# Optimization experiments

Measured on AMD Instinct MI355X. Metric: run time of the kernel, lower is better.

Reference implementation:

```python
import jax, jax.numpy as jnp
import numpy as np
import math

M = 8                      # multiplicity (channels per irrep)
COMBOS = [(0,0,0),(0,1,1),(1,0,1),(1,1,0),(1,1,1),(2,1,1)]  # (edge_l, node_l, out_l)

def _cg_coeff(j1, m1, j2, m2, j3, m3):
    # standard (Racah) complex Clebsch-Gordan coefficient <j1 m1 j2 m2 | j3 m3>
    if m3 != m1 + m2:
        return 0.0
    f = math.factorial
    vmin = max(0, j2 - j3 - m1, j1 + m2 - j3)
    vmax = min(j1 + j2 - j3, j1 - m1, j2 + m2)
    pref = (2*j3 + 1) * f(j3+j1-j2) * f(j3-j1+j2) * f(j1+j2-j3) / f(j1+j2+j3+1)
    pref *= f(j3+m3) * f(j3-m3) * f(j1-m1) * f(j1+m1) * f(j2-m2) * f(j2+m2)
    s = 0.0
    for v in range(vmin, vmax + 1):
        s += (-1)**v / (f(v) * f(j1+j2-j3-v) * f(j1-m1-v) * f(j2+m2-v)
                        * f(j3-j2+m1+v) * f(j3-j1-m2+v))
    return math.sqrt(pref) * s

def _su2_cg(l1, l2, l3):
    C = np.zeros((2*l1+1, 2*l2+1, 2*l3+1), dtype=np.complex128)
    for m1 in range(-l1, l1+1):
        for m2 in range(-l2, l2+1):
            m3 = m1 + m2
            if -l3 <= m3 <= l3:
                C[m1+l1, m2+l2, m3+l3] = _cg_coeff(l1, m1, l2, m2, l3, m3)
    return C

def _qmat(l):
    # real -> complex spherical-harmonic change of basis (e3nn convention)
    q = np.zeros((2*l+1, 2*l+1), dtype=np.complex128)
    for m in range(-l, 0):
        q[l+m, l+abs(m)] = 1/np.sqrt(2)
        q[l+m, l-abs(m)] = -1j/np.sqrt(2)
    q[l, l] = 1.0
    for m in range(1, l+1):
        q[l+m, l+abs(m)] = (-1)**m / np.sqrt(2)
        q[l+m, l-abs(m)] = 1j * (-1)**m / np.sqrt(2)
    return (-1j)**l * q

def _so3_cg(l1, l2, l3):
    # real-basis CG, normalized to unit Frobenius norm (matches e3nn _so3_clebsch_gordan)
    C = np.einsum('ij,kl,mn,ikn->jlm', _qmat(l1), _qmat(l2),
                  np.conj(_qmat(l3)).T, _su2_cg(l1, l2, l3))
    assert np.abs(C.imag).max() < 1e-6
    C = C.real
    return C / np.linalg.norm(C)

CG = {c: jnp.asarray(_so3_cg(*c), dtype=jnp.float32) for c in COMBOS}


def setup_inputs() -> dict:
    N, E = 100000, 1600000
    ks = jax.random.split(jax.random.key(0), 6)
    return {
        'node_irreps': jax.random.normal(ks[0], (N, 4*M), jnp.float32),
        'edge_index': jax.random.randint(ks[1], (2, E), 0, N, dtype=jnp.int32),
        'sh0': jax.random.normal(ks[2], (E, 1), jnp.float32),
        'sh1': jax.random.normal(ks[3], (E, 3), jnp.float32),
        'sh2': jax.random.normal(ks[4], (E, 5), jnp.float32),
        'W': jax.random.normal(ks[5], (len(COMBOS), M, M), jnp.float32),
    }


def reference(node_irreps, edge_index, sh0, sh1, sh2, W):
    N, E = node_irreps.shape[0], edge_index.shape[1]
    src = node_irreps[edge_index[0]]                    # gather: [E, 4M]
    feats = {0: src[:, :M][:, :, None],                 # scalar channels [E, M, 1]
             1: src[:, M:].reshape(E, M, 3)}            # vector channels [E, M, 3]
    sh = {0: sh0, 1: sh1, 2: sh2}
    msg = {0: jnp.zeros((E, M, 1), node_irreps.dtype),
           1: jnp.zeros((E, M, 3), node_irreps.dtype)}
    for idx, (le, ln, lo) in enumerate(COMBOS):
        # per-edge CG tensor product: [de,dn,do] x [E,de] x [E,M,dn] -> [E,M,do]
        base = jnp.einsum('ijk,ei,emj->emk', CG[(le, ln, lo)], sh[le], feats[ln])
        # channel-mixing scalar weights (in_channel -> out_channel)
        msg[lo] = msg[lo] + jnp.einsum('io,eik->eok', W[idx], base)
    tgt = edge_index[1]
    agg0 = jax.ops.segment_sum(msg[0].reshape(E, M), tgt, num_segments=N)     # [N, M]
    agg1 = jax.ops.segment_sum(msg[1].reshape(E, 3*M), tgt, num_segments=N)   # [N, 3M]
    return jnp.concatenate([agg0, agg1], axis=1)
```

## Files before the change

### kernel.cpp

```cpp
#include <hip/hip_runtime.h>

#define THREADS 256

typedef float v4f __attribute__((ext_vector_type(4)));
typedef int   v2i __attribute__((ext_vector_type(2)));


__global__ __launch_bounds__(THREADS) void k_hist2(const int* __restrict__ tgt,
                                                   int* __restrict__ cnt,
                                                   int* __restrict__ ke, int E) {
    int e = blockIdx.x * THREADS + threadIdx.x;
    if (e < E) ke[e] = atomicAdd(&cnt[tgt[e]], 1);
}

__global__ __launch_bounds__(THREADS) void k_hist(const int* __restrict__ tgt,
                                                  int* __restrict__ cnt, int E) {
    int e = blockIdx.x * THREADS + threadIdx.x;
    if (e < E) atomicAdd(&cnt[tgt[e]], 1);
}

__global__ __launch_bounds__(THREADS) void k_scan_partial(const int* __restrict__ cnt,
                                                          int* __restrict__ bsum, int N) {
    __shared__ int lds[THREADS];
    int base = blockIdx.x * 1024 + threadIdx.x * 4;
    int s = 0;
    #pragma unroll
    for (int k = 0; k < 4; ++k) { int i = base + k; if (i < N) s += cnt[i]; }
    lds[threadIdx.x] = s; __syncthreads();
    for (int off = THREADS / 2; off > 0; off >>= 1) {
        if (threadIdx.x < off) lds[threadIdx.x] += lds[threadIdx.x + off];
        __syncthreads();
    }
    if (threadIdx.x == 0) bsum[blockIdx.x] = lds[0];
}

__global__ __launch_bounds__(THREADS) void k_scan_final2(int* __restrict__ cnt,
                                                         const int* __restrict__ bsum,
                                                         int* __restrict__ rowptr,
                                                         int N, int E, int NB) {
    __shared__ int lbs[THREADS];
    __shared__ int lds[THREADS];
    const int t = threadIdx.x;

    lbs[t] = (t < NB) ? bsum[t] : 0;
    __syncthreads();
    for (int off = 1; off < THREADS; off <<= 1) {
        int x = (t >= off) ? lbs[t - off] : 0;
        __syncthreads();
        lbs[t] += x;
        __syncthreads();
    }
    const int chunkBase = (blockIdx.x > 0) ? lbs[blockIdx.x - 1] : 0;

    int base = blockIdx.x * 1024 + t * 4;
    int v[4]; int local = 0;
    #pragma unroll
    for (int k = 0; k < 4; ++k) {
        int i = base + k;
        v[k] = (i < N) ? cnt[i] : 0;
        local += v[k];
    }
    lds[t] = local; __syncthreads();
    for (int off = 1; off < THREADS; off <<= 1) {
        int x = (t >= off) ? lds[t - off] : 0;
        __syncthreads();
        lds[t] += x;
        __syncthreads();
    }
    int p = lds[t] - local + chunkBase;
    #pragma unroll
    for (int k = 0; k < 4; ++k) {
        int i = base + k;
        if (i < N) { rowptr[i] = p; cnt[i] = p; p += v[k]; }
    }
    if (blockIdx.x == 0 && t == 0) rowptr[N] = E;
}


__global__ __launch_bounds__(THREADS) void k_colscat2(const int* __restrict__ eidx,
                                                      const int* __restrict__ ke,
                                                      const int* __restrict__ rowptr,
                                                      int* __restrict__ cursor,
                                                      int* __restrict__ col2,
                                                      int E) {
    int e = blockIdx.x * THREADS + threadIdx.x;
    if (e >= E) return;
    const int src = eidx[e];
    const int tgt = eidx[E + e];
    int pos;
    if (ke) pos = rowptr[tgt] + ke[e];
    else    pos = atomicAdd(&cursor[tgt], 1);
    v2i v; v[0] = e; v[1] = src;
    *(v2i*)(col2 + 2*(size_t)pos) = v;
}


#define ACC_STRIDE 15

__global__ __launch_bounds__(THREADS) void k_agg9(const float* __restrict__ node,
                                                  const int*   __restrict__ rowptr,
                                                  const int*   __restrict__ col2,
                                                  const float* __restrict__ sh0,
                                                  const float* __restrict__ sh1,
                                                  const float* __restrict__ sh2,
                                                  const float* __restrict__ W,
                                                  float*       __restrict__ out,
                                                  int N) {
    __shared__ float sW[384];
    __shared__ float sAcc[32 * 8 * ACC_STRIDE];
    for (int t = threadIdx.x; t < 384; t += THREADS) sW[t] = W[t];
    __syncthreads();

    constexpr float IS3  = 0.57735026918962576f;
    constexpr float IS6  = 0.40824829046386302f;
    constexpr float IS10 = 0.31622776601683794f;
    constexpr float IS30 = 0.18257418583505536f;

    const int lane  = threadIdx.x & 63;
    const int wv    = threadIdx.x >> 6;
    const int i     = lane & 7;
    const int jslot = lane >> 3;

    for (int t = 0; t < 8; ++t) {
        const int n = blockIdx.x * 32 + wv * 8 + t;

        float a[14];
        #pragma unroll
        for (int k = 0; k < 14; ++k) a[k] = 0.f;

        if (n < N) {
            const int jbeg = rowptr[n];
            const int jend = rowptr[n + 1];

            if (jbeg < jend) {
                const int jlast = jend - 1;

                int j0  = jbeg + jslot;
                int jc0 = (j0 < jend) ? j0 : jlast;
                float mcur = (j0 < jend) ? 1.f : 0.f;
                v2i ec = *(const v2i*)(col2 + 2*(size_t)jc0);
                float s  = sh0[ec[0]];
                const float* up = sh1 + 3*(size_t)ec[0];
                float u0 = up[0], u1 = up[1], u2 = up[2];
                const float* qp = sh2 + 5*(size_t)ec[0];
                float q0 = qp[0], q1 = qp[1], q2 = qp[2], q3 = qp[3], q4 = qp[4];
                const float* nr = node + (size_t)ec[1] * 32;
                float f0 = nr[i];
                float x  = nr[8 + 3*i + 0];
                float y  = nr[8 + 3*i + 1];
                float z  = nr[8 + 3*i + 2];
                int j1  = jbeg + 8 + jslot;
                int jc1 = (j1 < jend) ? j1 : jlast;
                v2i ecn = *(const v2i*)(col2 + 2*(size_t)jc1);

                for (int g0 = jbeg; g0 < jend; g0 += 8) {
                    const int gn = g0 + 8;
                    const bool more = gn < jend;
                    float ns = 0.f, nu0 = 0.f, nu1 = 0.f, nu2 = 0.f;
                    float nq0 = 0.f, nq1 = 0.f, nq2 = 0.f, nq3 = 0.f, nq4 = 0.f;
                    float nf0 = 0.f, nx = 0.f, ny = 0.f, nz = 0.f;
                    float mnext = 0.f;
                    v2i ec2 = ecn;
                    if (more) {
                        mnext = (gn + jslot < jend) ? 1.f : 0.f;
                        ns = sh0[ecn[0]];
                        const float* nup = sh1 + 3*(size_t)ecn[0];
                        nu0 = nup[0]; nu1 = nup[1]; nu2 = nup[2];
                        const float* nqp = sh2 + 5*(size_t)ecn[0];
                        nq0 = nqp[0]; nq1 = nqp[1]; nq2 = nqp[2]; nq3 = nqp[3]; nq4 = nqp[4];
                        const float* nrn = node + (size_t)ecn[1] * 32;
                        nf0 = nrn[i];
                        nx  = nrn[8 + 3*i + 0];
                        ny  = nrn[8 + 3*i + 1];
                        nz  = nrn[8 + 3*i + 2];
                        int j2  = gn + 8 + jslot;
                        int jc2 = (j2 < jend) ? j2 : jlast;
                        ec2 = *(const v2i*)(col2 + 2*(size_t)jc2);
                    }

                    const float mf0 = f0 * mcur;
                    const float mx  = x  * mcur;
                    const float my  = y  * mcur;
                    const float mz  = z  * mcur;

                    const float Q00 = -q2*IS30 - q4*IS10;
                    const float Q01 =  q1*IS10;
                    const float Q02 =  q0*IS10;
                    const float Q11 =  2.0f*q2*IS30;
                    const float Q12 =  q3*IS10;
                    const float Q22 = -q2*IS30 + q4*IS10;

                    a[0]  += s * mf0;
                    a[1]  += u0*mx + u1*my + u2*mz;
                    a[2]  += s * mx;
                    a[3]  += s * my;
                    a[4]  += s * mz;
                    a[5]  += mf0 * u0;
                    a[6]  += mf0 * u1;
                    a[7]  += mf0 * u2;
                    a[8]  += u1*mz - u2*my;
                    a[9]  += u2*mx - u0*mz;
                    a[10] += u0*my - u1*mx;
                    a[11] += Q00*mx + Q01*my + Q02*mz;
                    a[12] += Q01*mx + Q11*my + Q12*mz;
                    a[13] += Q02*mx + Q12*my + Q22*mz;

                    if (more) {
                        s = ns; u0 = nu0; u1 = nu1; u2 = nu2;
                        q0 = nq0; q1 = nq1; q2 = nq2; q3 = nq3; q4 = nq4;
                        f0 = nf0; x = nx; y = ny; z = nz;
                        ecn = ec2; mcur = mnext;
                    }
                }
            }
        }

        #pragma unroll
        for (int k = 0; k < 14; ++k) {
            float v = a[k];
            v += __shfl_xor(v, 8);
            v += __shfl_xor(v, 16);
            v += __shfl_xor(v, 32);
            a[k] = v;
        }

        if (n < N && jslot == 0) {
            #pragma unroll
            for (int k = 1; k < 8; ++k) a[k] *= IS3;
            #pragma unroll
            for (int k = 8; k < 11; ++k) a[k] *= IS6;
            float* myAcc = &sAcc[((wv * 8 + t) * 8 + i) * ACC_STRIDE];
            #pragma unroll
            for (int k = 0; k < 14; ++k) myAcc[k] = a[k];
        }
    }
    __syncthreads();

    {
        const int nodeSlot = threadIdx.x >> 3;
        const int o        = threadIdx.x & 7;
        const int n        = blockIdx.x * 32 + nodeSlot;
        if (n < N) {
            float o0 = 0.f, ox = 0.f, oy = 0.f, oz = 0.f;
            #pragma unroll
            for (int ii = 0; ii < 8; ++ii) {
                const float* A = &sAcc[(nodeSlot * 8 + ii) * ACC_STRIDE];
                const float w0 = sW[  0 + ii*8 + o];
                const float w1 = sW[ 64 + ii*8 + o];
                const float w2 = sW[128 + ii*8 + o];
                const float w3 = sW[192 + ii*8 + o];
                const float w4 = sW[256 + ii*8 + o];
                const float w5 = sW[320 + ii*8 + o];
                o0 += w0*A[0]  + w3*A[1];
                ox += w1*A[2]  + w2*A[5] + w4*A[8]  + w5*A[11];
                oy += w1*A[3]  + w2*A[6] + w4*A[9]  + w5*A[12];
                oz += w1*A[4]  + w2*A[7] + w4*A[10] + w5*A[13];
            }
            float* orow = out + (size_t)n * 32;
            orow[o]         = o0;
            orow[8 + 3*o+0] = ox;
            orow[8 + 3*o+1] = oy;
            orow[8 + 3*o+2] = oz;
        }
    }
}


__global__ __launch_bounds__(THREADS) void msg_kernel_atomic(
    const float* __restrict__ node,
    const int*   __restrict__ eidx,
    const float* __restrict__ sh0,
    const float* __restrict__ sh1,
    const float* __restrict__ sh2,
    const float* __restrict__ W,
    float*       __restrict__ out,
    int E)
{
    __shared__ float sW[384];
    for (int t = threadIdx.x; t < 384; t += THREADS) sW[t] = W[t];
    __syncthreads();

    int e = blockIdx.x * THREADS + threadIdx.x;
    if (e >= E) return;

    constexpr float IS3  = 0.57735026918962576f;
    constexpr float IS6  = 0.40824829046386302f;
    constexpr float IS10 = 0.31622776601683794f;
    constexpr float IS30 = 0.18257418583505536f;

    const int src = eidx[e];
    const int tgt = eidx[E + e];

    const float s  = sh0[e];
    const float u0 = sh1[3*e+0], u1 = sh1[3*e+1], u2 = sh1[3*e+2];
    const float q0 = sh2[5*e+0], q1 = sh2[5*e+1], q2 = sh2[5*e+2],
                q3 = sh2[5*e+3], q4 = sh2[5*e+4];

    const float Q00 = -q2*IS30 - q4*IS10;
    const float Q01 =  q1*IS10;
    const float Q02 =  q0*IS10;
    const float Q11 =  2.0f*q2*IS30;
    const float Q12 =  q3*IS10;
    const float Q22 = -q2*IS30 + q4*IS10;

    float f[32];
    {
        const float4* nr = (const float4*)(node + (size_t)src * 32);
        #pragma unroll
        for (int i = 0; i < 8; ++i) {
            float4 v = nr[i];
            f[4*i+0]=v.x; f[4*i+1]=v.y; f[4*i+2]=v.z; f[4*i+3]=v.w;
        }
    }

    float msg[32];
    #pragma unroll
    for (int j = 0; j < 32; ++j) msg[j] = 0.0f;

    const float s13 = s * IS3;

    #pragma unroll
    for (int i = 0; i < 8; ++i) {
        const float f0i = f[i];
        const float x = f[8+3*i+0], y = f[8+3*i+1], z = f[8+3*i+2];
        const float c0  = s * f0i;
        const float c3  = IS3 * (u0*x + u1*y + u2*z);
        const float p2  = IS3 * f0i;
        const float c1x = s13*x, c1y = s13*y, c1z = s13*z;
        const float c2x = p2*u0, c2y = p2*u1, c2z = p2*u2;
        const float c4x = IS6*(u1*z - u2*y);
        const float c4y = IS6*(u2*x - u0*z);
        const float c4z = IS6*(u0*y - u1*x);
        const float c5x = Q00*x + Q01*y + Q02*z;
        const float c5y = Q01*x + Q11*y + Q12*z;
        const float c5z = Q02*x + Q12*y + Q22*z;

        float wr[6][8];
        #pragma unroll
        for (int c = 0; c < 6; ++c) {
            float4 aa = *(const float4*)&sW[c*64 + i*8 + 0];
            float4 bb = *(const float4*)&sW[c*64 + i*8 + 4];
            wr[c][0]=aa.x; wr[c][1]=aa.y; wr[c][2]=aa.z; wr[c][3]=aa.w;
            wr[c][4]=bb.x; wr[c][5]=bb.y; wr[c][6]=bb.z; wr[c][7]=bb.w;
        }

        #pragma unroll
        for (int o = 0; o < 8; ++o) {
            msg[o] += wr[0][o]*c0 + wr[3][o]*c3;
            msg[8+3*o+0] += wr[1][o]*c1x + wr[2][o]*c2x + wr[4][o]*c4x + wr[5][o]*c5x;
            msg[8+3*o+1] += wr[1][o]*c1y + wr[2][o]*c2y + wr[4][o]*c4y + wr[5][o]*c5y;
            msg[8+3*o+2] += wr[1][o]*c1z + wr[2][o]*c2z + wr[4][o]*c4z + wr[5][o]*c5z;
        }
    }

    float* orow = out + (size_t)tgt * 32;
    #pragma unroll
    for (int j = 0; j < 32; ++j) unsafeAtomicAdd(orow + j, msg[j]);
}


extern "C" void kernel_launch(void* const* d_in, const int* in_sizes, int n_in,
                              void* d_out, int out_size, void* d_ws, size_t ws_size,
                              hipStream_t stream) {
    const float* node = (const float*)d_in[0];
    const int*   eidx = (const int*)d_in[1];
    const float* sh0  = (const float*)d_in[2];
    const float* sh1  = (const float*)d_in[3];
    const float* sh2  = (const float*)d_in[4];
    const float* W    = (const float*)d_in[5];
    float* out = (float*)d_out;

    const int E = in_sizes[2];
    const int N = in_sizes[0] / 32;
    const int NB = (N + 1023) / 1024;

    size_t base_w = (size_t)N + (size_t)(N + 1) + 256;
    size_t intA_w = base_w + (size_t)E;
    size_t colA   = (intA_w + 3) & ~(size_t)3;
    size_t colB   = (base_w + 3) & ~(size_t)3;
    size_t needA  = (colA + 2*(size_t)E) * sizeof(float);
    size_t needB  = (colB + 2*(size_t)E) * sizeof(float);

    const int gridE = (E + THREADS - 1) / THREADS;

    if (ws_size >= needB && NB <= THREADS) {
        const bool useKe = (ws_size >= needA);

        int* wsI    = (int*)d_ws;
        int* cnt    = wsI;
        int* rowptr = cnt + N;
        int* bsum   = rowptr + (N + 1);
        int* ke     = useKe ? (bsum + 256) : nullptr;
        int* col2   = wsI + (useKe ? colA : colB);

        hipMemsetAsync(cnt, 0, (size_t)N * sizeof(int), stream);

        if (useKe)
            k_hist2<<<gridE, THREADS, 0, stream>>>(eidx + E, cnt, ke, E);
        else
            k_hist<<<gridE, THREADS, 0, stream>>>(eidx + E, cnt, E);

        k_scan_partial<<<NB, THREADS, 0, stream>>>(cnt, bsum, N);
        k_scan_final2<<<NB, THREADS, 0, stream>>>(cnt, bsum, rowptr, N, E, NB);

        k_colscat2<<<gridE, THREADS, 0, stream>>>(eidx, ke, rowptr, cnt, col2, E);

        k_agg9<<<(N + 31) / 32, THREADS, 0, stream>>>(node, rowptr, col2,
                                                      sh0, sh1, sh2, W, out, N);
    } else {
        hipMemsetAsync(d_out, 0, (size_t)out_size * sizeof(float), stream);
        msg_kernel_atomic<<<gridE, THREADS, 0, stream>>>(
            node, eidx, sh0, sh1, sh2, W, out, E);
    }
}
```

Baseline: 337.1 us.

## Pipeline edge gathers across node boundaries with deeper software prefetch in aggregation kernel

Rewrites the CSR aggregation kernel so each wavefront walks the edges of its 8 nodes as one continuous stream. A three-stage software pipeline keeps edge-index loads and operand gathers in flight across node boundaries, instead of draining the prefetch at the end of each node. Row pointers are loaded once into uniform registers, shared accumulators are zero-initialised so empty nodes need no special path, and launch bounds ask for 4 blocks per CU. The deeper pipeline holds more live registers, which may limit occupancy or cause spills, and the control flow for advancing between nodes is more complex.

```diff
diff --git a/kernel.cpp b/kernel.cpp
--- a/kernel.cpp
+++ b/kernel.cpp
@@ -97,19 +97,21 @@
 
 #define ACC_STRIDE 15
 
-__global__ __launch_bounds__(THREADS) void k_agg9(const float* __restrict__ node,
-                                                  const int*   __restrict__ rowptr,
-                                                  const int*   __restrict__ col2,
-                                                  const float* __restrict__ sh0,
-                                                  const float* __restrict__ sh1,
-                                                  const float* __restrict__ sh2,
-                                                  const float* __restrict__ W,
-                                                  float*       __restrict__ out,
-                                                  int N) {
+struct Ops { float s,u0,u1,u2,q0,q1,q2,q3,q4,f0,x,y,z; };
+
+__global__ __launch_bounds__(THREADS, 4)
+void k_agg10(const float* __restrict__ node,
+             const int*   __restrict__ rowptr,
+             const int*   __restrict__ col2,
+             const float* __restrict__ sh0,
+             const float* __restrict__ sh1,
+             const float* __restrict__ sh2,
+             const float* __restrict__ W,
+             float*       __restrict__ out,
+             int N) {
     __shared__ float sW[384];
     __shared__ float sAcc[32 * 8 * ACC_STRIDE];
     for (int t = threadIdx.x; t < 384; t += THREADS) sW[t] = W[t];
-    __syncthreads();
 
     constexpr float IS3  = 0.57735026918962576f;
     constexpr float IS6  = 0.40824829046386302f;
@@ -120,118 +122,128 @@
     const int wv    = threadIdx.x >> 6;
     const int i     = lane & 7;
     const int jslot = lane >> 3;
-
-    for (int t = 0; t < 8; ++t) {
-        const int n = blockIdx.x * 32 + wv * 8 + t;
-
-        float a[14];
+    const int nbase = blockIdx.x * 32 + wv * 8;
+
+    {
+        float* z = &sAcc[((wv * 8 + jslot) * 8 + i) * ACC_STRIDE];
         #pragma unroll
-        for (int k = 0; k < 14; ++k) a[k] = 0.f;
-
-        if (n < N) {
-            const int jbeg = rowptr[n];
-            const int jend = rowptr[n + 1];
-
-            if (jbeg < jend) {
-                const int jlast = jend - 1;
-
-                int j0  = jbeg + jslot;
-                int jc0 = (j0 < jend) ? j0 : jlast;
-                float mcur = (j0 < jend) ? 1.f : 0.f;
-                v2i ec = *(const v2i*)(col2 + 2*(size_t)jc0);
-                float s  = sh0[ec[0]];
-                const float* up = sh1 + 3*(size_t)ec[0];
-                float u0 = up[0], u1 = up[1], u2 = up[2];
-                const float* qp = sh2 + 5*(size_t)ec[0];
-                float q0 = qp[0], q1 = qp[1], q2 = qp[2], q3 = qp[3], q4 = qp[4];
-                const float* nr = node + (size_t)ec[1] * 32;
-                float f0 = nr[i];
-                float x  = nr[8 + 3*i + 0];
-                float y  = nr[8 + 3*i + 1];
-                float z  = nr[8 + 3*i + 2];
-                int j1  = jbeg + 8 + jslot;
-                int jc1 = (j1 < jend) ? j1 : jlast;
-                v2i ecn = *(const v2i*)(col2 + 2*(size_t)jc1);
-
-                for (int g0 = jbeg; g0 < jend; g0 += 8) {
-                    const int gn = g0 + 8;
-                    const bool more = gn < jend;
-                    float ns = 0.f, nu0 = 0.f, nu1 = 0.f, nu2 = 0.f;
-                    float nq0 = 0.f, nq1 = 0.f, nq2 = 0.f, nq3 = 0.f, nq4 = 0.f;
-                    float nf0 = 0.f, nx = 0.f, ny = 0.f, nz = 0.f;
-                    float mnext = 0.f;
-                    v2i ec2 = ecn;
-                    if (more) {
-                        mnext = (gn + jslot < jend) ? 1.f : 0.f;
-                        ns = sh0[ecn[0]];
-                        const float* nup = sh1 + 3*(size_t)ecn[0];
-                        nu0 = nup[0]; nu1 = nup[1]; nu2 = nup[2];
-                        const float* nqp = sh2 + 5*(size_t)ecn[0];
-                        nq0 = nqp[0]; nq1 = nqp[1]; nq2 = nqp[2]; nq3 = nqp[3]; nq4 = nqp[4];
-                        const float* nrn = node + (size_t)ecn[1] * 32;
-                        nf0 = nrn[i];
-                        nx  = nrn[8 + 3*i + 0];
-                        ny  = nrn[8 + 3*i + 1];
-                        nz  = nrn[8 + 3*i + 2];
-                        int j2  = gn + 8 + jslot;
-                        int jc2 = (j2 < jend) ? j2 : jlast;
-                        ec2 = *(const v2i*)(col2 + 2*(size_t)jc2);
-                    }
-
-                    const float mf0 = f0 * mcur;
-                    const float mx  = x  * mcur;
-                    const float my  = y  * mcur;
-                    const float mz  = z  * mcur;
-
-                    const float Q00 = -q2*IS30 - q4*IS10;
-                    const float Q01 =  q1*IS10;
-                    const float Q02 =  q0*IS10;
-                    const float Q11 =  2.0f*q2*IS30;
-                    const float Q12 =  q3*IS10;
-                    const float Q22 = -q2*IS30 + q4*IS10;
-
-                    a[0]  += s * mf0;
-                    a[1]  += u0*mx + u1*my + u2*mz;
-                    a[2]  += s * mx;
-                    a[3]  += s * my;
-                    a[4]  += s * mz;
-                    a[5]  += mf0 * u0;
-                    a[6]  += mf0 * u1;
-                    a[7]  += mf0 * u2;
-                    a[8]  += u1*mz - u2*my;
-                    a[9]  += u2*mx - u0*mz;
-                    a[10] += u0*my - u1*mx;
-                    a[11] += Q00*mx + Q01*my + Q02*mz;
-                    a[12] += Q01*mx + Q11*my + Q12*mz;
-                    a[13] += Q02*mx + Q12*my + Q22*mz;
-
-                    if (more) {
-                        s = ns; u0 = nu0; u1 = nu1; u2 = nu2;
-                        q0 = nq0; q1 = nq1; q2 = nq2; q3 = nq3; q4 = nq4;
-                        f0 = nf0; x = nx; y = ny; z = nz;
-                        ecn = ec2; mcur = mnext;
-                    }
+        for (int k = 0; k < 14; ++k) z[k] = 0.f;
+    }
+
+    int jb[9];
+    #pragma unroll
+    for (int k = 0; k < 9; ++k) {
+        int idx = nbase + k;
+        idx = (idx < N) ? idx : N;
+        jb[k] = __builtin_amdgcn_readfirstlane(rowptr[idx]);
+    }
+
+    float a[14];
+    #pragma unroll
+    for (int k = 0; k < 14; ++k) a[k] = 0.f;
+
+    auto ADV = [&](int& t, int& j) {
+        j += 8;
+        if (j >= jb[t + 1]) {
+            do { ++t; } while (t < 8 && jb[t] >= jb[t + 1]);
+            if (t < 8) j = jb[t];
+        }
+    };
+    auto PLOAD = [&](int t, int j, v2i& p, float& m) {
+        if (t < 8) {
+            int hi = jb[t + 1];
+            int jj = j + jslot;
+            int jc = (jj < hi) ? jj : hi - 1;
+            m = (jj < hi) ? 1.f : 0.f;
+            p = *(const v2i*)(col2 + 2 * (size_t)jc);
+        } else { m = 0.f; p[0] = 0; p[1] = 0; }
+    };
+    auto OLOAD = [&](const v2i& p, Ops& o) {
+        const int e = p[0], sr = p[1];
+        o.s = sh0[e];
+        const float* up = sh1 + 3 * (size_t)e;
+        o.u0 = up[0]; o.u1 = up[1]; o.u2 = up[2];
+        const float* qp = sh2 + 5 * (size_t)e;
+        o.q0 = qp[0]; o.q1 = qp[1]; o.q2 = qp[2]; o.q3 = qp[3]; o.q4 = qp[4];
+        const float* nr = node + (size_t)sr * 32;
+        o.f0 = nr[i];
+        o.x  = nr[8 + 3*i + 0];
+        o.y  = nr[8 + 3*i + 1];
+        o.z  = nr[8 + 3*i + 2];
+    };
+
+    int tA = 0;
+    while (tA < 8 && jb[tA] >= jb[tA + 1]) tA++;
+
+    if (tA < 8) {
+        int jA = jb[tA];
+        v2i pA; float mA; PLOAD(tA, jA, pA, mA);
+        Ops oA; OLOAD(pA, oA);
+        int tB = tA, jB = jA; ADV(tB, jB);
+        v2i pB; float mB; PLOAD(tB, jB, pB, mB);
+        Ops oB; OLOAD(pB, oB);
+        int tC = tB, jC = jB; if (tB < 8) ADV(tC, jC);
+        v2i pC; float mC; PLOAD(tC, jC, pC, mC);
+
+        while (tA < 8) {
+            Ops oC; OLOAD(pC, oC);
+            int tD = tC, jD = jC;
+            if (tC < 8) ADV(tD, jD);
+            v2i pD; float mD; PLOAD(tD, jD, pD, mD);
+
+            {
+                const float mf0 = oA.f0 * mA;
+                const float mx  = oA.x  * mA;
+                const float my  = oA.y  * mA;
+                const float mz  = oA.z  * mA;
+                const float Q00 = -oA.q2*IS30 - oA.q4*IS10;
+                const float Q01 =  oA.q1*IS10;
+                const float Q02 =  oA.q0*IS10;
+                const float Q11 =  2.0f*oA.q2*IS30;
+                const float Q12 =  oA.q3*IS10;
+                const float Q22 = -oA.q2*IS30 + oA.q4*IS10;
+
+                a[0]  += oA.s * mf0;
+                a[1]  += oA.u0*mx + oA.u1*my + oA.u2*mz;
+                a[2]  += oA.s * mx;
+                a[3]  += oA.s * my;
+                a[4]  += oA.s * mz;
+                a[5]  += mf0 * oA.u0;
+                a[6]  += mf0 * oA.u1;
+                a[7]  += mf0 * oA.u2;
+                a[8]  += oA.u1*mz - oA.u2*my;
+                a[9]  += oA.u2*mx - oA.u0*mz;
+                a[10] += oA.u0*my - oA.u1*mx;
+                a[11] += Q00*mx + Q01*my + Q02*mz;
+                a[12] += Q01*mx + Q11*my + Q12*mz;
+                a[13] += Q02*mx + Q12*my + Q22*mz;
+            }
+
+            if (jA + 8 >= jb[tA + 1]) {
+                #pragma unroll
+                for (int k = 0; k < 14; ++k) {
+                    float v = a[k];
+                    v += __shfl_xor(v, 8);
+                    v += __shfl_xor(v, 16);
+                    v += __shfl_xor(v, 32);
+                    a[k] = v;
                 }
+                if (jslot == 0) {
+                    #pragma unroll
+                    for (int k = 1; k < 8; ++k) a[k] *= IS3;
+                    #pragma unroll
+                    for (int k = 8; k < 11; ++k) a[k] *= IS6;
+                    float* myAcc = &sAcc[((wv * 8 + tA) * 8 + i) * ACC_STRIDE];
+                    #pragma unroll
+                    for (int k = 0; k < 14; ++k) myAcc[k] = a[k];
+                }
+                #pragma unroll
+                for (int k = 0; k < 14; ++k) a[k] = 0.f;
             }
-        }
-
-        #pragma unroll
-        for (int k = 0; k < 14; ++k) {
-            float v = a[k];
-            v += __shfl_xor(v, 8);
-            v += __shfl_xor(v, 16);
-            v += __shfl_xor(v, 32);
-            a[k] = v;
-        }
-
-        if (n < N && jslot == 0) {
-            #pragma unroll
-            for (int k = 1; k < 8; ++k) a[k] *= IS3;
-            #pragma unroll
-            for (int k = 8; k < 11; ++k) a[k] *= IS6;
-            float* myAcc = &sAcc[((wv * 8 + t) * 8 + i) * ACC_STRIDE];
-            #pragma unroll
-            for (int k = 0; k < 14; ++k) myAcc[k] = a[k];
+
+            tA = tB; jA = jB; oA = oB; mA = mB;
+            tB = tC; jB = jC; oB = oC; mB = mC;
+            tC = tD; jC = jD; pC = pD; mC = mD;
         }
     }
     __syncthreads();
@@ -405,8 +417,8 @@
 
         k_colscat2<<<gridE, THREADS, 0, stream>>>(eidx, ke, rowptr, cnt, col2, E);
 
-        k_agg9<<<(N + 31) / 32, THREADS, 0, stream>>>(node, rowptr, col2,
-                                                      sh0, sh1, sh2, W, out, N);
+        k_agg10<<<(N + 31) / 32, THREADS, 0, stream>>>(node, rowptr, col2,
+                                                       sh0, sh1, sh2, W, out, N);
     } else {
         hipMemsetAsync(d_out, 0, (size_t)out_size * sizeof(float), stream);
         msg_kernel_atomic<<<gridE, THREADS, 0, stream>>>(
```

Result: slower. 370.8 us (+10.0%).
